# Optimization experiments

Measured on AMD Instinct MI355X. Metric: run time of the kernel, lower is better.

## Reference

```python
import jax, jax.numpy as jnp
import numpy as np

D_MODEL = 256
D_INNER = 512   # expand=2
D_STATE = 16
D_CONV = 4
DT_RANK = 16    # ceil(d_model/16)
EPS = 1e-5


def _ln(x, g, b):
    m = x.mean(-1, keepdims=True)
    v = jnp.mean((x - m) ** 2, -1, keepdims=True)
    return (x - m) * jax.lax.rsqrt(v + EPS) * g + b


def _mamba(x, W_in, conv_w, conv_b, W_x, W_dt, b_dt, A_log, Dp, W_out):
    B, N, _ = x.shape
    xz = x @ W_in.T                               # [B,N,2*Di]
    xs, z = jnp.split(xz, 2, axis=-1)
    # depthwise causal conv1d, kernel D_CONV, left pad D_CONV-1
    xp = jnp.pad(xs, ((0, 0), (D_CONV - 1, 0), (0, 0)))
    xc = sum(xp[:, k:k + N, :] * conv_w[:, k] for k in range(D_CONV)) + conv_b
    xc = jax.nn.silu(xc)                          # [B,N,Di]
    dbl = xc @ W_x.T                              # [B,N,dt_rank+2*S]
    dt, Bm, Cm = jnp.split(dbl, [DT_RANK, DT_RANK + D_STATE], axis=-1)
    dt = jax.nn.softplus(dt @ W_dt.T + b_dt)      # [B,N,Di]
    A = -jnp.exp(A_log)                           # [Di,S]
    dA = jnp.exp(dt[..., None] * A)               # [B,N,Di,S]
    dBx = dt[..., None] * Bm[:, :, None, :] * xc[..., None]

    def step(h, inp):
        dA_t, dBx_t, c_t = inp                    # [B,Di,S],[B,Di,S],[B,S]
        h = dA_t * h + dBx_t
        y = jnp.einsum('bds,bs->bd', h, c_t)
        return h, y

    h0 = jnp.zeros((B, D_INNER, D_STATE), xs.dtype)
    _, ys = jax.lax.scan(step, h0, (dA.swapaxes(0, 1), dBx.swapaxes(0, 1), Cm.swapaxes(0, 1)))
    y = ys.swapaxes(0, 1) + Dp * xc
    y = y * jax.nn.silu(z)
    return y @ W_out.T                            # [B,N,d_model]


def setup_inputs() -> dict:
    key = jax.random.key(0)
    ks = jax.random.split(key, 24)
    g = lambda k, s, sc=0.02: jax.random.normal(k, s, jnp.float32) * sc
    inp = {}
    inp['input_states'] = jax.random.normal(ks[0], (1, 8192, D_MODEL), jnp.float32)
    inp['position_states'] = jax.random.normal(ks[1], (1, 8192, D_MODEL), jnp.float32)
    inp['W_in'] = g(ks[2], (2 * D_INNER, D_MODEL))
    inp['conv_w'] = g(ks[3], (D_INNER, D_CONV), 0.2)
    inp['conv_b'] = jnp.zeros((D_INNER,), jnp.float32)
    inp['W_x'] = g(ks[4], (DT_RANK + 2 * D_STATE, D_INNER))
    inp['W_dt'] = g(ks[5], (D_INNER, DT_RANK), 0.1)
    inp['b_dt'] = g(ks[6], (D_INNER,), 0.1)
    # S4D-real init: A_log = log(1..d_state) broadcast over channels
    inp['A_log'] = jnp.log(jnp.broadcast_to(jnp.arange(1, D_STATE + 1, dtype=jnp.float32), (D_INNER, D_STATE)))
    inp['Dp'] = jnp.ones((D_INNER,), jnp.float32)
    inp['W_out'] = g(ks[7], (D_MODEL, D_INNER))
    inp['W_lin'] = g(ks[8], (D_MODEL, D_MODEL))
    inp['b_lin'] = jnp.zeros((D_MODEL,), jnp.float32)
    inp['ln1_g'] = jnp.ones((D_MODEL,), jnp.float32)
    inp['ln1_b'] = jnp.zeros((D_MODEL,), jnp.float32)
    inp['W_exp'] = g(ks[9], (2 * D_MODEL, D_MODEL))
    inp['b_exp'] = jnp.zeros((2 * D_MODEL,), jnp.float32)
    inp['W_sq'] = g(ks[10], (D_MODEL, 2 * D_MODEL))
    inp['b_sq'] = jnp.zeros((D_MODEL,), jnp.float32)
    inp['ln2_g'] = jnp.ones((D_MODEL,), jnp.float32)
    inp['ln2_b'] = jnp.zeros((D_MODEL,), jnp.float32)
    return inp


def reference(input_states, position_states, W_in, conv_w, conv_b, W_x, W_dt, b_dt,
              A_log, Dp, W_out, W_lin, b_lin, ln1_g, ln1_b, W_exp, b_exp, W_sq, b_sq,
              ln2_g, ln2_b):
    h = _mamba(input_states, W_in, conv_w, conv_b, W_x, W_dt, b_dt, A_log, Dp, W_out)
    h = h @ W_lin.T + b_lin
    h = _ln(h + input_states, ln1_g, ln1_b)
    ff = jax.nn.relu(h @ W_exp.T + b_exp) @ W_sq.T + b_sq
    out = _ln(h + ff, ln2_g, ln2_b)
    # RPEMamba returns (hidden, input_states) as (states, attention_scores)
    return out, input_states
```

## Files before the change

kernel.cpp:

```cpp
#include <hip/hip_runtime.h>
#include <stdint.h>

#define NT 8192
#define DM 256
#define DI 512
#define DS 16
#define DR 16
#define NCH 512
#define LCH 16
#define NSUP 32
#define CPS 16

typedef __bf16 bf16_t;
typedef bf16_t bf16x8 __attribute__((ext_vector_type(8)));
typedef float f32x4 __attribute__((ext_vector_type(4)));

__device__ __forceinline__ unsigned short f2b(float f) {
    union { float f; unsigned int i; } v; v.f = f;
    unsigned int r = v.i + 0x7fffu + ((v.i >> 16) & 1u);
    return (unsigned short)(r >> 16);
}
__device__ __forceinline__ bf16x8 ld_frag_lds(const unsigned short* p) {
    union { uint4 u; bf16x8 b; } v;
    v.u = *(const uint4*)p;
    return v.b;
}
__device__ __forceinline__ void async16(const unsigned short* g, unsigned short* l) {
    __builtin_amdgcn_global_load_lds(
        (const __attribute__((address_space(1))) unsigned int*)g,
        (__attribute__((address_space(3))) unsigned int*)l, 16, 0, 0);
}
__device__ __forceinline__ float fast_softplus(float x) {
    return x > 20.f ? x : __logf(1.f + __expf(x));
}
__device__ __forceinline__ float silu(float x) {
    return x / (1.f + __expf(-x));
}

struct CvtArgs {
    const float* src[7];
    unsigned short* dst[7];
    int cnt[7];
    int total;
};
__global__ __launch_bounds__(256) void cvt_all(CvtArgs a) {
    int i = blockIdx.x * 256 + threadIdx.x;
    if (i >= a.total) return;
    #pragma unroll
    for (int s = 0; s < 7; s++) {
        if (i < a.cnt[s]) { a.dst[s][i] = f2b(a.src[s][i]); return; }
        i -= a.cnt[s];
    }
}

template<int BM, int BN, int FLAGS>
__global__ __launch_bounds__(256) void gemm_lds(
    const unsigned short* __restrict__ A, const unsigned short* __restrict__ B,
    int M, int N, int K,
    const float* __restrict__ bias, const float* __restrict__ resid,
    float* __restrict__ Cf, unsigned short* __restrict__ Cb)
{
    constexpr int MI = BM / 32;
    constexpr int NJ = BN / 32;
    __shared__ unsigned short sA[BM * 64];
    __shared__ unsigned short sB[BN * 64];
    const int tid = threadIdx.x;
    const int m0 = blockIdx.x * BM;
    const int n0 = blockIdx.y * BN;
    const int wave = tid >> 6, lane = tid & 63;
    const int wm = (wave & 1) * (BM / 2);
    const int wn = (wave >> 1) * (BN / 2);
    const int qm = lane >> 4, rm = lane & 15;

    f32x4 acc[MI][NJ];
    #pragma unroll
    for (int i = 0; i < MI; i++)
        #pragma unroll
        for (int j = 0; j < NJ; j++)
            #pragma unroll
            for (int r = 0; r < 4; r++) acc[i][j][r] = 0.f;

    const int sr = tid >> 3;
    const int sc = (tid & 7) * 8;

    for (int k0 = 0; k0 < K; k0 += 64) {
        __syncthreads();
        #pragma unroll
        for (int j = 0; j < BM / 32; j++) {
            int r = sr + j * 32;
            async16(A + (size_t)(m0 + r) * K + k0 + sc, &sA[r * 64 + sc]);
        }
        #pragma unroll
        for (int j = 0; j < BN / 32; j++) {
            int r = sr + j * 32;
            if (n0 + r < N)
                async16(B + (size_t)(n0 + r) * K + k0 + sc, &sB[r * 64 + sc]);
        }
        __syncthreads();
        #pragma unroll
        for (int ks = 0; ks < 64; ks += 32) {
            bf16x8 af[MI], bfr[NJ];
            #pragma unroll
            for (int i = 0; i < MI; i++)
                af[i] = ld_frag_lds(&sA[(wm + i * 16 + rm) * 64 + ks + qm * 8]);
            #pragma unroll
            for (int j = 0; j < NJ; j++)
                bfr[j] = ld_frag_lds(&sB[(wn + j * 16 + rm) * 64 + ks + qm * 8]);
            #pragma unroll
            for (int i = 0; i < MI; i++)
                #pragma unroll
                for (int j = 0; j < NJ; j++)
                    acc[i][j] = __builtin_amdgcn_mfma_f32_16x16x32_bf16(
                        af[i], bfr[j], acc[i][j], 0, 0, 0);
        }
    }

    #pragma unroll
    for (int i = 0; i < MI; i++) {
        int mrow = m0 + wm + i * 16 + qm * 4;
        #pragma unroll
        for (int j = 0; j < NJ; j++) {
            int ncol = n0 + wn + j * 16 + rm;
            if (ncol < N) {
                #pragma unroll
                for (int r = 0; r < 4; r++) {
                    float v = acc[i][j][r];
                    int mm = mrow + r;
                    if constexpr (FLAGS & 1) v += bias[ncol];
                    if constexpr (FLAGS & 4) v += resid[(size_t)mm * N + ncol];
                    if constexpr (FLAGS & 2) v = v > 0.f ? v : 0.f;
                    if constexpr (FLAGS & 8) Cf[(size_t)mm * N + ncol] = v;
                    if constexpr (FLAGS & 16) Cb[(size_t)mm * N + ncol] = f2b(v);
                }
            }
        }
    }
}

__global__ __launch_bounds__(256) void conv_silu_b(
    const float* __restrict__ xz, const float* __restrict__ cw,
    const float* __restrict__ cb, unsigned short* __restrict__ xcb)
{
    int idx = blockIdx.x * 256 + threadIdx.x;
    int d = idx & (DI - 1), t = idx >> 9;
    float v = cb[d];
    #pragma unroll
    for (int k = 0; k < 4; k++) {
        int tt = t - 3 + k;
        if (tt >= 0) v += xz[(size_t)tt * 1024 + d] * cw[d * 4 + k];
    }
    xcb[idx] = f2b(silu(v));
}

__global__ __launch_bounds__(256, 4) void scan1(
    const float* __restrict__ xz, const float* __restrict__ cw,
    const float* __restrict__ cbp, const float* __restrict__ dbl,
    const float* __restrict__ Wdt, const float* __restrict__ bdt,
    const float* __restrict__ A_log,
    float* __restrict__ Ac, float* __restrict__ Bc)
{
    __shared__ float sR[LCH * 48];
    const int d = blockIdx.x * 256 + threadIdx.x;
    const int c = blockIdx.y;
    const int t0 = c * LCH;
    {
        const float4* src = (const float4*)(dbl + (size_t)t0 * 48);
        if (threadIdx.x < 192) ((float4*)sR)[threadIdx.x] = src[threadIdx.x];
    }
    __syncthreads();
    const float cw0 = cw[d*4], cw1 = cw[d*4+1], cw2 = cw[d*4+2], cw3 = cw[d*4+3];
    const float cb = cbp[d];
    const float* xzp = xz + d;
    float x0 = (t0 >= 3) ? xzp[(size_t)(t0-3) * 1024] : 0.f;
    float x1 = (t0 >= 2) ? xzp[(size_t)(t0-2) * 1024] : 0.f;
    float x2 = (t0 >= 1) ? xzp[(size_t)(t0-1) * 1024] : 0.f;
    float w[DR], A[DS], h[DS];
    #pragma unroll
    for (int j = 0; j < DR; j++) w[j] = Wdt[d * DR + j];
    const float bd = bdt[d];
    #pragma unroll
    for (int s = 0; s < DS; s++) { A[s] = -__expf(A_log[d * DS + s]); h[s] = 0.f; }
    float sumdt = 0.f;
    #pragma unroll 4
    for (int t = 0; t < LCH; t++) {
        float x3 = xzp[(size_t)(t0 + t) * 1024];
        float cv = cb + x0 * cw0 + x1 * cw1 + x2 * cw2 + x3 * cw3;
        x0 = x1; x1 = x2; x2 = x3;
        float xcv = silu(cv);
        const float* r = &sR[t * 48];
        float4 rd[4], rb[4];
        #pragma unroll
        for (int k = 0; k < 4; k++) { rd[k] = ((const float4*)r)[k]; rb[k] = ((const float4*)r)[4 + k]; }
        float accd = bd;
        #pragma unroll
        for (int k = 0; k < 4; k++)
            accd += rd[k].x * w[4*k] + rd[k].y * w[4*k+1] + rd[k].z * w[4*k+2] + rd[k].w * w[4*k+3];
        float dtv = fast_softplus(accd);
        sumdt += dtv;
        float dtx = dtv * xcv;
        const float* bptr = (const float*)rb;
        #pragma unroll
        for (int s = 0; s < DS; s++)
            h[s] = __expf(dtv * A[s]) * h[s] + dtx * bptr[s];
    }
    #pragma unroll
    for (int s = 0; s < DS; s++) {
        size_t off = ((size_t)c * DS + s) * DI + d;
        Ac[off] = __expf(sumdt * A[s]);
        Bc[off] = h[s];
    }
}

__global__ __launch_bounds__(256) void scan2a(
    const float* __restrict__ Ac, const float* __restrict__ Bc,
    float* __restrict__ Ap, float* __restrict__ Hl,
    float* __restrict__ Es, float* __restrict__ Ds)
{
    int p = blockIdx.x * 256 + threadIdx.x;
    int j = blockIdx.y;
    float h = 0.f, P = 1.f;
    for (int cc = 0; cc < CPS; cc++) {
        size_t off = (size_t)(j * CPS + cc) * 8192 + p;
        Hl[off] = h; Ap[off] = P;
        float a = Ac[off];
        h = a * h + Bc[off];
        P *= a;
    }
    Es[(size_t)j * 8192 + p] = h;
    Ds[(size_t)j * 8192 + p] = P;
}

__global__ __launch_bounds__(256) void scan2b(
    const float* __restrict__ Es, const float* __restrict__ Ds,
    float* __restrict__ Ss)
{
    int p = blockIdx.x * 256 + threadIdx.x;
    float S = 0.f;
    for (int j = 0; j < NSUP; j++) {
        Ss[(size_t)j * 8192 + p] = S;
        S = Ds[(size_t)j * 8192 + p] * S + Es[(size_t)j * 8192 + p];
    }
}

__global__ __launch_bounds__(256, 4) void scan3(
    const float* __restrict__ xz, const float* __restrict__ cw,
    const float* __restrict__ cbp, const float* __restrict__ dbl,
    const float* __restrict__ Wdt, const float* __restrict__ bdt,
    const float* __restrict__ A_log, const float* __restrict__ Dpp,
    const float* __restrict__ Ap, const float* __restrict__ Hl,
    const float* __restrict__ Ss, unsigned short* __restrict__ ygb)
{
    __shared__ float sR[LCH * 48];
    const int d = blockIdx.x * 256 + threadIdx.x;
    const int c = blockIdx.y;
    const int jsup = c / CPS;
    const int t0 = c * LCH;
    {
        const float4* src = (const float4*)(dbl + (size_t)t0 * 48);
        if (threadIdx.x < 192) ((float4*)sR)[threadIdx.x] = src[threadIdx.x];
    }
    __syncthreads();
    const float cw0 = cw[d*4], cw1 = cw[d*4+1], cw2 = cw[d*4+2], cw3 = cw[d*4+3];
    const float cb = cbp[d];
    const float* xzp = xz + d;
    const float* zp  = xz + DI + d;
    float x0 = (t0 >= 3) ? xzp[(size_t)(t0-3) * 1024] : 0.f;
    float x1 = (t0 >= 2) ? xzp[(size_t)(t0-2) * 1024] : 0.f;
    float x2 = (t0 >= 1) ? xzp[(size_t)(t0-1) * 1024] : 0.f;
    float w[DR], A[DS], h[DS];
    #pragma unroll
    for (int j = 0; j < DR; j++) w[j] = Wdt[d * DR + j];
    const float bd = bdt[d];
    const float dpv = Dpp[d];
    #pragma unroll
    for (int s = 0; s < DS; s++) {
        A[s] = -__expf(A_log[d * DS + s]);
        size_t off = (size_t)c * 8192 + s * DI + d;
        h[s] = Ap[off] * Ss[(size_t)jsup * 8192 + s * DI + d] + Hl[off];
    }
    #pragma unroll 4
    for (int t = 0; t < LCH; t++) {
        float x3 = xzp[(size_t)(t0 + t) * 1024];
        float zv = zp[(size_t)(t0 + t) * 1024];
        float cv = cb + x0 * cw0 + x1 * cw1 + x2 * cw2 + x3 * cw3;
        x0 = x1; x1 = x2; x2 = x3;
        float xcv = silu(cv);
        const float* r = &sR[t * 48];
        float4 rd[4], rb[4], rc[4];
        #pragma unroll
        for (int k = 0; k < 4; k++) {
            rd[k] = ((const float4*)r)[k];
            rb[k] = ((const float4*)r)[4 + k];
            rc[k] = ((const float4*)r)[8 + k];
        }
        float accd = bd;
        #pragma unroll
        for (int k = 0; k < 4; k++)
            accd += rd[k].x * w[4*k] + rd[k].y * w[4*k+1] + rd[k].z * w[4*k+2] + rd[k].w * w[4*k+3];
        float dtv = fast_softplus(accd);
        float dtx = dtv * xcv;
        const float* bptr = (const float*)rb;
        const float* cptr = (const float*)rc;
        float y = 0.f;
        #pragma unroll
        for (int s = 0; s < DS; s++) {
            h[s] = __expf(dtv * A[s]) * h[s] + dtx * bptr[s];
            y += h[s] * cptr[s];
        }
        ygb[(size_t)(t0 + t) * DI + d] = f2b((y + dpv * xcv) * silu(zv));
    }
}

__global__ __launch_bounds__(256) void lnorm(
    const float* __restrict__ X, const float* __restrict__ X2,
    const float* __restrict__ g, const float* __restrict__ b,
    float* __restrict__ outf, unsigned short* __restrict__ outb,
    const float* __restrict__ csrc, float* __restrict__ cdst)
{
    int wave = threadIdx.x >> 6, lane = threadIdx.x & 63;
    int row = blockIdx.x * 4 + wave;
    const float* x = X + (size_t)row * DM;
    float v[4];
    #pragma unroll
    for (int i = 0; i < 4; i++) {
        int col = lane + i * 64;
        v[i] = x[col];
        if (X2) v[i] += X2[(size_t)row * DM + col];
    }
    if (cdst) {
        #pragma unroll
        for (int i = 0; i < 4; i++) {
            int col = lane + i * 64;
            cdst[(size_t)row * DM + col] = csrc[(size_t)row * DM + col];
        }
    }
    float s = v[0] + v[1] + v[2] + v[3];
    float s2 = v[0]*v[0] + v[1]*v[1] + v[2]*v[2] + v[3]*v[3];
    #pragma unroll
    for (int m = 1; m < 64; m <<= 1) {
        s  += __shfl_xor(s, m, 64);
        s2 += __shfl_xor(s2, m, 64);
    }
    float mean = s * (1.f / DM);
    float var = s2 * (1.f / DM) - mean * mean;
    float inv = rsqrtf(var + 1e-5f);
    #pragma unroll
    for (int i = 0; i < 4; i++) {
        int col = lane + i * 64;
        float o = (v[i] - mean) * inv * g[col] + b[col];
        if (outf) outf[(size_t)row * DM + col] = o;
        if (outb) outb[(size_t)row * DM + col] = f2b(o);
    }
}

static constexpr size_t OFF_XZ    = 0;
static constexpr size_t OFF_XCB   = 33554432;
static constexpr size_t OFF_DBL   = 41943040;
static constexpr size_t OFF_AC    = 43515904;
static constexpr size_t OFF_BC    = 60293120;
static constexpr size_t OFF_HL    = 77070336;
static constexpr size_t OFF_AP    = 93847552;
static constexpr size_t OFF_ES    = 110624768;
static constexpr size_t OFF_DS2   = 111673344;
static constexpr size_t OFF_SS    = 112721920;
static constexpr size_t OFF_YGB   = 113770496;
static constexpr size_t OFF_XB    = 122159104;
static constexpr size_t OFF_WINB  = 126353408;
static constexpr size_t OFF_WXB   = 126877696;
static constexpr size_t OFF_WOUTB = 126926848;
static constexpr size_t OFF_WLINB = 127188992;
static constexpr size_t OFF_WEXPB = 127320064;
static constexpr size_t OFF_WSQB  = 127582208;
static constexpr size_t OFF_H1B   = OFF_AC;
static constexpr size_t OFF_H2    = OFF_AC + 4194304;
static constexpr size_t OFF_HLN   = OFF_BC;
static constexpr size_t OFF_HLNB  = OFF_BC + 8388608;
static constexpr size_t OFF_FF1B  = OFF_HL;
static constexpr size_t OFF_FF2   = OFF_AP;

extern "C" void kernel_launch(void* const* d_in, const int* in_sizes, int n_in,
                              void* d_out, int out_size, void* d_ws, size_t ws_size,
                              hipStream_t stream)
{
    const float* x      = (const float*)d_in[0];
    const float* W_in   = (const float*)d_in[2];
    const float* conv_w = (const float*)d_in[3];
    const float* conv_b = (const float*)d_in[4];
    const float* W_x    = (const float*)d_in[5];
    const float* W_dt   = (const float*)d_in[6];
    const float* b_dt   = (const float*)d_in[7];
    const float* A_log  = (const float*)d_in[8];
    const float* Dp     = (const float*)d_in[9];
    const float* W_out  = (const float*)d_in[10];
    const float* W_lin  = (const float*)d_in[11];
    const float* b_lin  = (const float*)d_in[12];
    const float* ln1_g  = (const float*)d_in[13];
    const float* ln1_b  = (const float*)d_in[14];
    const float* W_exp  = (const float*)d_in[15];
    const float* b_exp  = (const float*)d_in[16];
    const float* W_sq   = (const float*)d_in[17];
    const float* b_sq   = (const float*)d_in[18];
    const float* ln2_g  = (const float*)d_in[19];
    const float* ln2_b  = (const float*)d_in[20];

    char* ws = (char*)d_ws;
    float* xz   = (float*)(ws + OFF_XZ);
    unsigned short* xcb = (unsigned short*)(ws + OFF_XCB);
    float* dbl  = (float*)(ws + OFF_DBL);
    float* Ac   = (float*)(ws + OFF_AC);
    float* Bc   = (float*)(ws + OFF_BC);
    float* Hl   = (float*)(ws + OFF_HL);
    float* Ap   = (float*)(ws + OFF_AP);
    float* Es   = (float*)(ws + OFF_ES);
    float* Ds   = (float*)(ws + OFF_DS2);
    float* Ss   = (float*)(ws + OFF_SS);
    unsigned short* ygb   = (unsigned short*)(ws + OFF_YGB);
    unsigned short* xb    = (unsigned short*)(ws + OFF_XB);
    unsigned short* winb  = (unsigned short*)(ws + OFF_WINB);
    unsigned short* wxb   = (unsigned short*)(ws + OFF_WXB);
    unsigned short* woutb = (unsigned short*)(ws + OFF_WOUTB);
    unsigned short* wlinb = (unsigned short*)(ws + OFF_WLINB);
    unsigned short* wexpb = (unsigned short*)(ws + OFF_WEXPB);
    unsigned short* wsqb  = (unsigned short*)(ws + OFF_WSQB);
    unsigned short* h1b   = (unsigned short*)(ws + OFF_H1B);
    float* h2   = (float*)(ws + OFF_H2);
    float* hln  = (float*)(ws + OFF_HLN);
    unsigned short* hlnb  = (unsigned short*)(ws + OFF_HLNB);
    unsigned short* ff1b  = (unsigned short*)(ws + OFF_FF1B);
    float* ff2  = (float*)(ws + OFF_FF2);
    float* outp = (float*)d_out;

    CvtArgs ca;
    ca.src[0] = x;     ca.dst[0] = xb;    ca.cnt[0] = NT * DM;
    ca.src[1] = W_in;  ca.dst[1] = winb;  ca.cnt[1] = 1024 * DM;
    ca.src[2] = W_x;   ca.dst[2] = wxb;   ca.cnt[2] = 48 * DI;
    ca.src[3] = W_out; ca.dst[3] = woutb; ca.cnt[3] = DM * DI;
    ca.src[4] = W_lin; ca.dst[4] = wlinb; ca.cnt[4] = DM * DM;
    ca.src[5] = W_exp; ca.dst[5] = wexpb; ca.cnt[5] = DI * DM;
    ca.src[6] = W_sq;  ca.dst[6] = wsqb;  ca.cnt[6] = DM * DI;
    ca.total = ca.cnt[0]+ca.cnt[1]+ca.cnt[2]+ca.cnt[3]+ca.cnt[4]+ca.cnt[5]+ca.cnt[6];
    cvt_all<<<(ca.total + 255) / 256, 256, 0, stream>>>(ca);

    gemm_lds<128,128,8><<<dim3(64, 8), 256, 0, stream>>>(xb, winb, NT, 1024, DM,
                                                         nullptr, nullptr, xz, nullptr);
    conv_silu_b<<<NT * DI / 256, 256, 0, stream>>>(xz, conv_w, conv_b, xcb);
    gemm_lds<128,64,8><<<dim3(64, 1), 256, 0, stream>>>(xcb, wxb, NT, 48, DI,
                                                        nullptr, nullptr, dbl, nullptr);
    scan1<<<dim3(2, NCH), 256, 0, stream>>>(xz, conv_w, conv_b, dbl, W_dt, b_dt,
                                            A_log, Ac, Bc);
    scan2a<<<dim3(32, NSUP), 256, 0, stream>>>(Ac, Bc, Ap, Hl, Es, Ds);
    scan2b<<<32, 256, 0, stream>>>(Es, Ds, Ss);
    scan3<<<dim3(2, NCH), 256, 0, stream>>>(xz, conv_w, conv_b, dbl, W_dt, b_dt,
                                            A_log, Dp, Ap, Hl, Ss, ygb);
    gemm_lds<64,128,16><<<dim3(128, 2), 256, 0, stream>>>(ygb, woutb, NT, DM, DI,
                                                          nullptr, nullptr, nullptr, h1b);
    gemm_lds<64,128,1|4|8><<<dim3(128, 2), 256, 0, stream>>>(h1b, wlinb, NT, DM, DM,
                                                             b_lin, x, h2, nullptr);
    lnorm<<<NT / 4, 256, 0, stream>>>(h2, nullptr, ln1_g, ln1_b, hln, hlnb,
                                      nullptr, nullptr);
    gemm_lds<128,128,1|2|16><<<dim3(64, 4), 256, 0, stream>>>(hlnb, wexpb, NT, DI, DM,
                                                              b_exp, nullptr, nullptr, ff1b);
    gemm_lds<64,128,1|8><<<dim3(128, 2), 256, 0, stream>>>(ff1b, wsqb, NT, DM, DI,
                                                           b_sq, nullptr, ff2, nullptr);
    lnorm<<<NT / 4, 256, 0, stream>>>(hln, ff2, ln2_g, ln2_b, outp, nullptr,
                                      x, outp + (size_t)NT * DM);
}
```

Baseline: 289.4 us.

## Fold W_out into W_lin, store xz as bf16, retune GEMM tiles

W_lin and W_out are pre-multiplied into one combined weight, using a transposed W_out written during conversion, so the out-projection and linear GEMMs collapse into one GEMM with bias and residual. The in-projection output xz is now stored as bf16 instead of fp32, halving the traffic read by conv and both scan kernels. Several GEMM tile shapes and grids are also changed to raise block counts. The costs are an extra small GEMM per call, bf16 rounding of the combined weight and of xz, and a possible accuracy change.

```diff
diff --git a/kernel.cpp b/kernel.cpp
--- a/kernel.cpp
+++ b/kernel.cpp
@@ -20,6 +20,9 @@
     unsigned int r = v.i + 0x7fffu + ((v.i >> 16) & 1u);
     return (unsigned short)(r >> 16);
 }
+__device__ __forceinline__ float b2f(unsigned short u) {
+    union { unsigned int i; float f; } v; v.i = ((unsigned int)u) << 16; return v.f;
+}
 __device__ __forceinline__ bf16x8 ld_frag_lds(const unsigned short* p) {
     union { uint4 u; bf16x8 b; } v;
     v.u = *(const uint4*)p;
@@ -48,7 +51,16 @@
     if (i >= a.total) return;
     #pragma unroll
     for (int s = 0; s < 7; s++) {
-        if (i < a.cnt[s]) { a.dst[s][i] = f2b(a.src[s][i]); return; }
+        if (i < a.cnt[s]) {
+            unsigned short v = f2b(a.src[s][i]);
+            if (s == 3) {
+                int k = i >> 9, j = i & 511;
+                a.dst[s][j * 256 + k] = v;
+            } else {
+                a.dst[s][i] = v;
+            }
+            return;
+        }
         i -= a.cnt[s];
     }
 }
@@ -138,7 +150,7 @@
 }
 
 __global__ __launch_bounds__(256) void conv_silu_b(
-    const float* __restrict__ xz, const float* __restrict__ cw,
+    const unsigned short* __restrict__ xz, const float* __restrict__ cw,
     const float* __restrict__ cb, unsigned short* __restrict__ xcb)
 {
     int idx = blockIdx.x * 256 + threadIdx.x;
@@ -147,13 +159,13 @@
     #pragma unroll
     for (int k = 0; k < 4; k++) {
         int tt = t - 3 + k;
-        if (tt >= 0) v += xz[(size_t)tt * 1024 + d] * cw[d * 4 + k];
+        if (tt >= 0) v += b2f(xz[(size_t)tt * 1024 + d]) * cw[d * 4 + k];
     }
     xcb[idx] = f2b(silu(v));
 }
 
 __global__ __launch_bounds__(256, 4) void scan1(
-    const float* __restrict__ xz, const float* __restrict__ cw,
+    const unsigned short* __restrict__ xz, const float* __restrict__ cw,
     const float* __restrict__ cbp, const float* __restrict__ dbl,
     const float* __restrict__ Wdt, const float* __restrict__ bdt,
     const float* __restrict__ A_log,
@@ -170,10 +182,10 @@
     __syncthreads();
     const float cw0 = cw[d*4], cw1 = cw[d*4+1], cw2 = cw[d*4+2], cw3 = cw[d*4+3];
     const float cb = cbp[d];
-    const float* xzp = xz + d;
-    float x0 = (t0 >= 3) ? xzp[(size_t)(t0-3) * 1024] : 0.f;
-    float x1 = (t0 >= 2) ? xzp[(size_t)(t0-2) * 1024] : 0.f;
-    float x2 = (t0 >= 1) ? xzp[(size_t)(t0-1) * 1024] : 0.f;
+    const unsigned short* xzp = xz + d;
+    float x0 = (t0 >= 3) ? b2f(xzp[(size_t)(t0-3) * 1024]) : 0.f;
+    float x1 = (t0 >= 2) ? b2f(xzp[(size_t)(t0-2) * 1024]) : 0.f;
+    float x2 = (t0 >= 1) ? b2f(xzp[(size_t)(t0-1) * 1024]) : 0.f;
     float w[DR], A[DS], h[DS];
     #pragma unroll
     for (int j = 0; j < DR; j++) w[j] = Wdt[d * DR + j];
@@ -183,7 +195,7 @@
     float sumdt = 0.f;
     #pragma unroll 4
     for (int t = 0; t < LCH; t++) {
-        float x3 = xzp[(size_t)(t0 + t) * 1024];
+        float x3 = b2f(xzp[(size_t)(t0 + t) * 1024]);
         float cv = cb + x0 * cw0 + x1 * cw1 + x2 * cw2 + x3 * cw3;
         x0 = x1; x1 = x2; x2 = x3;
         float xcv = silu(cv);
@@ -243,7 +255,7 @@
 }
 
 __global__ __launch_bounds__(256, 4) void scan3(
-    const float* __restrict__ xz, const float* __restrict__ cw,
+    const unsigned short* __restrict__ xz, const float* __restrict__ cw,
     const float* __restrict__ cbp, const float* __restrict__ dbl,
     const float* __restrict__ Wdt, const float* __restrict__ bdt,
     const float* __restrict__ A_log, const float* __restrict__ Dpp,
@@ -262,11 +274,11 @@
     __syncthreads();
     const float cw0 = cw[d*4], cw1 = cw[d*4+1], cw2 = cw[d*4+2], cw3 = cw[d*4+3];
     const float cb = cbp[d];
-    const float* xzp = xz + d;
-    const float* zp  = xz + DI + d;
-    float x0 = (t0 >= 3) ? xzp[(size_t)(t0-3) * 1024] : 0.f;
-    float x1 = (t0 >= 2) ? xzp[(size_t)(t0-2) * 1024] : 0.f;
-    float x2 = (t0 >= 1) ? xzp[(size_t)(t0-1) * 1024] : 0.f;
+    const unsigned short* xzp = xz + d;
+    const unsigned short* zp  = xz + DI + d;
+    float x0 = (t0 >= 3) ? b2f(xzp[(size_t)(t0-3) * 1024]) : 0.f;
+    float x1 = (t0 >= 2) ? b2f(xzp[(size_t)(t0-2) * 1024]) : 0.f;
+    float x2 = (t0 >= 1) ? b2f(xzp[(size_t)(t0-1) * 1024]) : 0.f;
     float w[DR], A[DS], h[DS];
     #pragma unroll
     for (int j = 0; j < DR; j++) w[j] = Wdt[d * DR + j];
@@ -280,8 +292,8 @@
     }
     #pragma unroll 4
     for (int t = 0; t < LCH; t++) {
-        float x3 = xzp[(size_t)(t0 + t) * 1024];
-        float zv = zp[(size_t)(t0 + t) * 1024];
+        float x3 = b2f(xzp[(size_t)(t0 + t) * 1024]);
+        float zv = b2f(zp[(size_t)(t0 + t) * 1024]);
         float cv = cb + x0 * cw0 + x1 * cw1 + x2 * cw2 + x3 * cw3;
         x0 = x1; x1 = x2; x2 = x3;
         float xcv = silu(cv);
@@ -353,26 +365,26 @@
     }
 }
 
-static constexpr size_t OFF_XZ    = 0;
-static constexpr size_t OFF_XCB   = 33554432;
-static constexpr size_t OFF_DBL   = 41943040;
-static constexpr size_t OFF_AC    = 43515904;
-static constexpr size_t OFF_BC    = 60293120;
-static constexpr size_t OFF_HL    = 77070336;
-static constexpr size_t OFF_AP    = 93847552;
-static constexpr size_t OFF_ES    = 110624768;
-static constexpr size_t OFF_DS2   = 111673344;
-static constexpr size_t OFF_SS    = 112721920;
-static constexpr size_t OFF_YGB   = 113770496;
-static constexpr size_t OFF_XB    = 122159104;
-static constexpr size_t OFF_WINB  = 126353408;
-static constexpr size_t OFF_WXB   = 126877696;
-static constexpr size_t OFF_WOUTB = 126926848;
-static constexpr size_t OFF_WLINB = 127188992;
-static constexpr size_t OFF_WEXPB = 127320064;
-static constexpr size_t OFF_WSQB  = 127582208;
-static constexpr size_t OFF_H1B   = OFF_AC;
-static constexpr size_t OFF_H2    = OFF_AC + 4194304;
+static constexpr size_t OFF_XZB   = 0;
+static constexpr size_t OFF_XCB   = 16777216;
+static constexpr size_t OFF_DBL   = 25165824;
+static constexpr size_t OFF_AC    = 26738688;
+static constexpr size_t OFF_BC    = 43515904;
+static constexpr size_t OFF_HL    = 60293120;
+static constexpr size_t OFF_AP    = 77070336;
+static constexpr size_t OFF_ES    = 93847552;
+static constexpr size_t OFF_DS2   = 94896128;
+static constexpr size_t OFF_SS    = 95944704;
+static constexpr size_t OFF_YGB   = 96993280;
+static constexpr size_t OFF_XB    = 105381888;
+static constexpr size_t OFF_WINB  = 109576192;
+static constexpr size_t OFF_WXB   = 110100480;
+static constexpr size_t OFF_WOUTT = 110149632;
+static constexpr size_t OFF_WLINB = 110411776;
+static constexpr size_t OFF_WEXPB = 110542848;
+static constexpr size_t OFF_WSQB  = 110804992;
+static constexpr size_t OFF_WCOMB = 111067136;
+static constexpr size_t OFF_H2    = OFF_AC;
 static constexpr size_t OFF_HLN   = OFF_BC;
 static constexpr size_t OFF_HLNB  = OFF_BC + 8388608;
 static constexpr size_t OFF_FF1B  = OFF_HL;
@@ -404,7 +416,7 @@
     const float* ln2_b  = (const float*)d_in[20];
 
     char* ws = (char*)d_ws;
-    float* xz   = (float*)(ws + OFF_XZ);
+    unsigned short* xzb = (unsigned short*)(ws + OFF_XZB);
     unsigned short* xcb = (unsigned short*)(ws + OFF_XCB);
     float* dbl  = (float*)(ws + OFF_DBL);
     float* Ac   = (float*)(ws + OFF_AC);
@@ -418,11 +430,11 @@
     unsigned short* xb    = (unsigned short*)(ws + OFF_XB);
     unsigned short* winb  = (unsigned short*)(ws + OFF_WINB);
     unsigned short* wxb   = (unsigned short*)(ws + OFF_WXB);
-    unsigned short* woutb = (unsigned short*)(ws + OFF_WOUTB);
+    unsigned short* woutT = (unsigned short*)(ws + OFF_WOUTT);
     unsigned short* wlinb = (unsigned short*)(ws + OFF_WLINB);
     unsigned short* wexpb = (unsigned short*)(ws + OFF_WEXPB);
     unsigned short* wsqb  = (unsigned short*)(ws + OFF_WSQB);
-    unsigned short* h1b   = (unsigned short*)(ws + OFF_H1B);
+    unsigned short* wcomb = (unsigned short*)(ws + OFF_WCOMB);
     float* h2   = (float*)(ws + OFF_H2);
     float* hln  = (float*)(ws + OFF_HLN);
     unsigned short* hlnb  = (unsigned short*)(ws + OFF_HLNB);
@@ -434,34 +446,34 @@
     ca.src[0] = x;     ca.dst[0] = xb;    ca.cnt[0] = NT * DM;
     ca.src[1] = W_in;  ca.dst[1] = winb;  ca.cnt[1] = 1024 * DM;
     ca.src[2] = W_x;   ca.dst[2] = wxb;   ca.cnt[2] = 48 * DI;
-    ca.src[3] = W_out; ca.dst[3] = woutb; ca.cnt[3] = DM * DI;
+    ca.src[3] = W_out; ca.dst[3] = woutT; ca.cnt[3] = DM * DI;
     ca.src[4] = W_lin; ca.dst[4] = wlinb; ca.cnt[4] = DM * DM;
     ca.src[5] = W_exp; ca.dst[5] = wexpb; ca.cnt[5] = DI * DM;
     ca.src[6] = W_sq;  ca.dst[6] = wsqb;  ca.cnt[6] = DM * DI;
     ca.total = ca.cnt[0]+ca.cnt[1]+ca.cnt[2]+ca.cnt[3]+ca.cnt[4]+ca.cnt[5]+ca.cnt[6];
     cvt_all<<<(ca.total + 255) / 256, 256, 0, stream>>>(ca);
 
-    gemm_lds<128,128,8><<<dim3(64, 8), 256, 0, stream>>>(xb, winb, NT, 1024, DM,
-                                                         nullptr, nullptr, xz, nullptr);
-    conv_silu_b<<<NT * DI / 256, 256, 0, stream>>>(xz, conv_w, conv_b, xcb);
-    gemm_lds<128,64,8><<<dim3(64, 1), 256, 0, stream>>>(xcb, wxb, NT, 48, DI,
+    gemm_lds<64,64,16><<<dim3(4, 8), 256, 0, stream>>>(wlinb, woutT, DM, DI, DM,
+                                                       nullptr, nullptr, nullptr, wcomb);
+    gemm_lds<128,128,16><<<dim3(64, 8), 256, 0, stream>>>(xb, winb, NT, 1024, DM,
+                                                          nullptr, nullptr, nullptr, xzb);
+    conv_silu_b<<<NT * DI / 256, 256, 0, stream>>>(xzb, conv_w, conv_b, xcb);
+    gemm_lds<64,64,8><<<dim3(128, 1), 256, 0, stream>>>(xcb, wxb, NT, 48, DI,
                                                         nullptr, nullptr, dbl, nullptr);
-    scan1<<<dim3(2, NCH), 256, 0, stream>>>(xz, conv_w, conv_b, dbl, W_dt, b_dt,
+    scan1<<<dim3(2, NCH), 256, 0, stream>>>(xzb, conv_w, conv_b, dbl, W_dt, b_dt,
                                             A_log, Ac, Bc);
     scan2a<<<dim3(32, NSUP), 256, 0, stream>>>(Ac, Bc, Ap, Hl, Es, Ds);
     scan2b<<<32, 256, 0, stream>>>(Es, Ds, Ss);
-    scan3<<<dim3(2, NCH), 256, 0, stream>>>(xz, conv_w, conv_b, dbl, W_dt, b_dt,
+    scan3<<<dim3(2, NCH), 256, 0, stream>>>(xzb, conv_w, conv_b, dbl, W_dt, b_dt,
                                             A_log, Dp, Ap, Hl, Ss, ygb);
-    gemm_lds<64,128,16><<<dim3(128, 2), 256, 0, stream>>>(ygb, woutb, NT, DM, DI,
-                                                          nullptr, nullptr, nullptr, h1b);
-    gemm_lds<64,128,1|4|8><<<dim3(128, 2), 256, 0, stream>>>(h1b, wlinb, NT, DM, DM,
-                                                             b_lin, x, h2, nullptr);
+    gemm_lds<64,64,1|4|8><<<dim3(128, 4), 256, 0, stream>>>(ygb, wcomb, NT, DM, DI,
+                                                            b_lin, x, h2, nullptr);
     lnorm<<<NT / 4, 256, 0, stream>>>(h2, nullptr, ln1_g, ln1_b, hln, hlnb,
                                       nullptr, nullptr);
-    gemm_lds<128,128,1|2|16><<<dim3(64, 4), 256, 0, stream>>>(hlnb, wexpb, NT, DI, DM,
+    gemm_lds<64,128,1|2|16><<<dim3(128, 4), 256, 0, stream>>>(hlnb, wexpb, NT, DI, DM,
                                                               b_exp, nullptr, nullptr, ff1b);
-    gemm_lds<64,128,1|8><<<dim3(128, 2), 256, 0, stream>>>(ff1b, wsqb, NT, DM, DI,
-                                                           b_sq, nullptr, ff2, nullptr);
+    gemm_lds<64,64,1|8><<<dim3(128, 4), 256, 0, stream>>>(ff1b, wsqb, NT, DM, DI,
+                                                          b_sq, nullptr, ff2, nullptr);
     lnorm<<<NT / 4, 256, 0, stream>>>(hln, ff2, ln2_g, ln2_b, outp, nullptr,
                                       x, outp + (size_t)NT * DM);
 }
```

After: 286.1 us. No clear change (-1.1%).
